# Kernel tuning notes

Hardware: AMD Instinct MI355X
Metric: run time of the kernel (lower is better)

## Reference

```python
import jax, jax.numpy as jnp
import numpy as np

NUM_CLASSES = 21
NUM_BOXES = 8732
BATCH = 128


def setup_inputs() -> dict:
    key = jax.random.key(0)
    k1, k2, k3, k4 = jax.random.split(key, 4)
    return {
        "loc_preds": jax.random.normal(k1, (BATCH, NUM_BOXES, 4), dtype=jnp.float32),
        "loc_targets": jax.random.normal(k2, (BATCH, NUM_BOXES, 4), dtype=jnp.float32),
        "conf_preds": jax.random.normal(k3, (BATCH, NUM_BOXES, NUM_CLASSES), dtype=jnp.float32),
        "label_targets": jax.random.randint(k4, (BATCH, NUM_BOXES), 0, NUM_CLASSES, dtype=jnp.int64),
    }


def reference(loc_preds, loc_targets, conf_preds, label_targets):
    n, num_boxes, _ = conf_preds.shape
    pos = label_targets > 0                                   # [n, B] matched boxes
    num_matched = jnp.sum(pos).astype(conf_preds.dtype)

    # --- localization loss: smooth L1 (beta=1) summed over positive boxes ---
    diff = loc_preds - loc_targets
    ad = jnp.abs(diff)
    sl1 = jnp.where(ad < 1.0, 0.5 * diff * diff, ad - 0.5)    # [n, B, 4]
    loc_loss = jnp.sum(jnp.where(pos[:, :, None], sl1, 0.0))

    # --- per-box CE for mining (original uses a single global max for logsumexp) ---
    x_max = jax.lax.stop_gradient(jnp.max(conf_preds))
    lse = jnp.log(jnp.sum(jnp.exp(conf_preds - x_max), axis=-1)) + x_max   # [n, B]
    gold = jnp.take_along_axis(conf_preds, label_targets[..., None], axis=-1)[..., 0]
    mining_loss = jnp.where(pos, -1.0, lse - gold)            # pos boxes forced lowest

    # --- hard negative mining: double argsort -> rank of each box's loss ---
    idx = jnp.argsort(-mining_loss, axis=1)                   # descending sort indices
    rank = jnp.argsort(idx, axis=1)                           # rank of each box
    num_pos = jnp.sum(pos.astype(jnp.int32), axis=1)          # [n]
    num_neg = jnp.minimum(3 * num_pos, num_boxes - 1)         # [n]
    neg = rank < num_neg[:, None]
    sel = pos | neg                                           # [n, B]

    # --- confidence loss: standard CE over selected boxes (F.cross_entropy) ---
    logp = jax.nn.log_softmax(conf_preds, axis=-1)
    ce = -jnp.take_along_axis(logp, label_targets[..., None], axis=-1)[..., 0]
    conf_loss = jnp.sum(jnp.where(sel, ce, 0.0))

    denom = jnp.maximum(num_matched, 1.0)
    return (loc_loss + conf_loss) / denom
```

## Files before the change

### kernel.cpp

```cpp
#include <hip/hip_runtime.h>

#define NB 8732
#define NC 21
#define BATCH 128
#define BX 35

#define WS_ROW (BATCH * BX * 4)

__device__ inline float wred_f(float v) {
#pragma unroll
    for (int o = 32; o > 0; o >>= 1) v += __shfl_down(v, o, 64);
    return v;
}

__global__ void __launch_bounds__(256)
kA(const float* __restrict__ locp, const float* __restrict__ loct,
   const float* __restrict__ conf, const int* __restrict__ lab,
   float* __restrict__ ws) {
    __shared__ float xb[4][1344];
    const int r = blockIdx.y;
    const int w = threadIdx.x >> 6;
    const int ln = threadIdx.x & 63;
    const int box0 = blockIdx.x * 256 + w * 64;

    float ceS = 0.f, pceS = 0.f, llS = 0.f, npS = 0.f;

    if (box0 < NB) {
        const int cnt = min(64, NB - box0);
        const size_t rowbase = (size_t)r * NB;
        const float* __restrict__ src = conf + (rowbase + box0) * (size_t)NC;

        int l = 0;
        float4 lp = {0.f, 0.f, 0.f, 0.f}, lt = {0.f, 0.f, 0.f, 0.f};
        if (ln < cnt) {
            const size_t box = rowbase + box0 + ln;
            l = lab[box];
            lp = *(const float4*)(locp + box * 4);
            lt = *(const float4*)(loct + box * 4);
        }

        if (cnt == 64) {
            float v[21];
#pragma unroll
            for (int j = 0; j < 21; j++) v[j] = src[64 * j + ln];
#pragma unroll
            for (int j = 0; j < 21; j++) xb[w][64 * j + ln] = v[j];
        } else {
            const int nflat = cnt * NC;
#pragma unroll
            for (int j = 0; j < 21; j++) {
                const int idx = 64 * j + ln;
                if (idx < nflat) xb[w][idx] = src[idx];
            }
        }
        asm volatile("s_waitcnt lgkmcnt(0)" ::: "memory");

        if (ln < cnt) {
            float c[21];
            const float* bp = &xb[w][21 * ln];
#pragma unroll
            for (int j = 0; j < 21; j++) c[j] = bp[j];
            float m = c[0];
#pragma unroll
            for (int j = 1; j < 21; j++) m = fmaxf(m, c[j]);
            float s = 0.f;
#pragma unroll
            for (int j = 0; j < 21; j++) s += __expf(c[j] - m);
            float gold = c[0];
#pragma unroll
            for (int j = 1; j < 21; j++) gold = (j == l) ? c[j] : gold;
            const float ce = m + __logf(s) - gold;
            ceS = ce;
            if (l > 0) {
                npS = 1.f;
                pceS = ce;
                float d, ad;
                d = lp.x - lt.x; ad = fabsf(d); llS += (ad < 1.f) ? 0.5f * d * d : ad - 0.5f;
                d = lp.y - lt.y; ad = fabsf(d); llS += (ad < 1.f) ? 0.5f * d * d : ad - 0.5f;
                d = lp.z - lt.z; ad = fabsf(d); llS += (ad < 1.f) ? 0.5f * d * d : ad - 0.5f;
                d = lp.w - lt.w; ad = fabsf(d); llS += (ad < 1.f) ? 0.5f * d * d : ad - 0.5f;
            }
        }
    }

    __shared__ float sr[4][4];
    float v0 = wred_f(ceS), v1 = wred_f(pceS), v2 = wred_f(llS), v3 = wred_f(npS);
    if (ln == 0) { sr[0][w] = v0; sr[1][w] = v1; sr[2][w] = v2; sr[3][w] = v3; }
    __syncthreads();
    if (threadIdx.x == 0) {
        float A = 0, B = 0, C = 0, D = 0;
#pragma unroll
        for (int k = 0; k < 4; k++) { A += sr[0][k]; B += sr[1][k]; C += sr[2][k]; D += sr[3][k]; }
        float* slot = ws + ((size_t)r * BX + blockIdx.x) * 4;
        slot[0] = A; slot[1] = B; slot[2] = C; slot[3] = D;
    }
}

__device__ inline float ce_for_box0(const float* __restrict__ cp) {
    float c[NC];
#pragma unroll
    for (int j = 0; j < NC; j++) c[j] = cp[j];
    float m = c[0];
#pragma unroll
    for (int j = 1; j < NC; j++) m = fmaxf(m, c[j]);
    float s = 0.f;
#pragma unroll
    for (int j = 0; j < NC; j++) s += __expf(c[j] - m);
    return m + __logf(s) - c[0];
}

__global__ void __launch_bounds__(256)
kB(const float* __restrict__ conf, const int* __restrict__ lab,
   float* __restrict__ ws) {
    const int r = blockIdx.x;
    __shared__ float srow[4];
    if (threadIdx.x < 64) {
        float a = 0, b = 0, c = 0, d = 0;
        if (threadIdx.x < BX) {
            const float4 p = *(const float4*)(ws + ((size_t)r * BX + threadIdx.x) * 4);
            a = p.x; b = p.y; c = p.z; d = p.w;
        }
        a = wred_f(a); b = wred_f(b); c = wred_f(c); d = wred_f(d);
        if (threadIdx.x == 0) { srow[0] = a; srow[1] = b; srow[2] = c; srow[3] = d; }
    }
    __syncthreads();
    const float row_ce = srow[0], row_pce = srow[1], row_ll = srow[2];
    const int np = (int)srow[3];
    const int K = min(3 * np, NB - 1);
    const int nneg = NB - np;

    float rowval;
    if (K >= nneg) {
        rowval = row_ce;
    } else if (K <= 0) {
        rowval = row_pce;
    } else {
        __shared__ unsigned key[NB];
        __shared__ unsigned hist[256];
        __shared__ unsigned sb[2];
        for (int i = threadIdx.x; i < NB; i += 256) {
            const size_t box = (size_t)r * NB + i;
            unsigned k = 0u;
            if (lab[box] == 0) {
                float ce = ce_for_box0(conf + box * (size_t)NC);
                k = __float_as_uint(fmaxf(ce, 0.f));
            }
            key[i] = k;
        }
        __syncthreads();
        unsigned prefix = 0;
        int Kr = K;
        for (int round = 3; round >= 0; --round) {
            const int sh = round * 8;
            const unsigned pmask = (round == 3) ? 0u : (0xFFFFFFFFu << (8 * (round + 1)));
            for (int b = threadIdx.x; b < 256; b += 256) hist[b] = 0;
            __syncthreads();
            for (int i = threadIdx.x; i < NB; i += 256) {
                const unsigned k = key[i];
                if ((k & pmask) == prefix) atomicAdd(&hist[(k >> sh) & 255u], 1u);
            }
            __syncthreads();
            if (threadIdx.x == 0) {
                unsigned cum = 0; int b = 255;
                for (; b > 0; --b) {
                    const unsigned h = hist[b];
                    if (cum + h >= (unsigned)Kr) break;
                    cum += h;
                }
                sb[0] = cum; sb[1] = (unsigned)b;
            }
            __syncthreads();
            Kr -= (int)sb[0];
            prefix |= (sb[1] << sh);
            __syncthreads();
        }
        float local = 0.f;
        for (int i = threadIdx.x; i < NB; i += 256) {
            const unsigned k = key[i];
            if (k > prefix) local += __uint_as_float(k);
        }
        __shared__ float sred[4];
        float v = wred_f(local);
        const int ww = threadIdx.x >> 6, lnn = threadIdx.x & 63;
        if (lnn == 0) sred[ww] = v;
        __syncthreads();
        rowval = row_pce + sred[0] + sred[1] + sred[2] + sred[3]
               + (float)Kr * __uint_as_float(prefix);
    }

    if (threadIdx.x == 0) {
        float* o = ws + WS_ROW + r * 4;
        o[0] = rowval; o[1] = row_ll; o[2] = srow[3];
    }
}

__global__ void __launch_bounds__(256)
kC(const float* __restrict__ ws, float* __restrict__ out) {
    float cf = 0.f, lc = 0.f, nm = 0.f;
    if (threadIdx.x < BATCH) {
        const float* o = ws + WS_ROW + threadIdx.x * 4;
        cf = o[0]; lc = o[1]; nm = o[2];
    }
    __shared__ float sf[4], sl[4], sn[4];
    float vc = wred_f(cf), vl = wred_f(lc), vn = wred_f(nm);
    const int w = threadIdx.x >> 6, ln = threadIdx.x & 63;
    if (ln == 0) { sf[w] = vc; sl[w] = vl; sn[w] = vn; }
    __syncthreads();
    if (threadIdx.x == 0) {
        const float CF = sf[0] + sf[1] + sf[2] + sf[3];
        const float LC = sl[0] + sl[1] + sl[2] + sl[3];
        const float NM = sn[0] + sn[1] + sn[2] + sn[3];
        out[0] = (LC + CF) / fmaxf(NM, 1.f);
    }
}

extern "C" void kernel_launch(void* const* d_in, const int* in_sizes, int n_in,
                              void* d_out, int out_size, void* d_ws, size_t ws_size,
                              hipStream_t stream) {
    const float* locp = (const float*)d_in[0];
    const float* loct = (const float*)d_in[1];
    const float* conf = (const float*)d_in[2];
    const int* lab = (const int*)d_in[3];
    float* out = (float*)d_out;
    float* ws = (float*)d_ws;

    hipLaunchKernelGGL(kA, dim3(BX, BATCH), dim3(256), 0, stream,
                       locp, loct, conf, lab, ws);
    hipLaunchKernelGGL(kB, dim3(BATCH), dim3(256), 0, stream, conf, lab, ws);
    hipLaunchKernelGGL(kC, dim3(1), dim3(256), 0, stream, ws, out);
}
```

Baseline: 176.2 us.

## Make kA persistent per row with double-buffered register prefetch of chunks

The grid of kA shrinks from 35 to 7 blocks per row. Each wave now loops over 64-box chunks with a stride of 28 waves, and it prefetches the next chunk's confidence, label and loc data into registers while the current chunk goes through shared memory and the CE computation. The goal is to hide global-load latency and cut per-block overhead and the number of partial sums kB must reduce. In exchange the kernel uses more registers, since launch_bounds(256,4) and two 21-float buffers raise spill risk, and the grid is smaller with only 896 blocks, so latency hiding depends on the software pipeline.

```diff
diff --git a/kernel.cpp b/kernel.cpp
--- a/kernel.cpp
+++ b/kernel.cpp
@@ -3,9 +3,10 @@
 #define NB 8732
 #define NC 21
 #define BATCH 128
-#define BX 35
-
-#define WS_ROW (BATCH * BX * 4)
+#define BXS 7
+#define WPR 28
+#define STRIDE (WPR * 64)
+#define WS_ROW (BATCH * BXS * 4)
 
 __device__ inline float wred_f(float v) {
 #pragma unroll
@@ -13,7 +14,7 @@
     return v;
 }
 
-__global__ void __launch_bounds__(256)
+__global__ void __launch_bounds__(256, 4)
 kA(const float* __restrict__ locp, const float* __restrict__ loct,
    const float* __restrict__ conf, const int* __restrict__ lab,
    float* __restrict__ ws) {
@@ -21,77 +22,116 @@
     const int r = blockIdx.y;
     const int w = threadIdx.x >> 6;
     const int ln = threadIdx.x & 63;
-    const int box0 = blockIdx.x * 256 + w * 64;
+    float* X = xb[w];
+    const int wid = blockIdx.x * 4 + w;
+    const size_t rowbase = (size_t)r * NB;
+    const float* __restrict__ crow = conf + rowbase * NC;
 
     float ceS = 0.f, pceS = 0.f, llS = 0.f, npS = 0.f;
 
-    if (box0 < NB) {
-        const int cnt = min(64, NB - box0);
-        const size_t rowbase = (size_t)r * NB;
-        const float* __restrict__ src = conf + (rowbase + box0) * (size_t)NC;
-
-        int l = 0;
-        float4 lp = {0.f, 0.f, 0.f, 0.f}, lt = {0.f, 0.f, 0.f, 0.f};
-        if (ln < cnt) {
-            const size_t box = rowbase + box0 + ln;
-            l = lab[box];
-            lp = *(const float4*)(locp + box * 4);
-            lt = *(const float4*)(loct + box * 4);
-        }
-
-        if (cnt == 64) {
-            float v[21];
-#pragma unroll
-            for (int j = 0; j < 21; j++) v[j] = src[64 * j + ln];
-#pragma unroll
-            for (int j = 0; j < 21; j++) xb[w][64 * j + ln] = v[j];
-        } else {
-            const int nflat = cnt * NC;
-#pragma unroll
-            for (int j = 0; j < 21; j++) {
-                const int idx = 64 * j + ln;
-                if (idx < nflat) xb[w][idx] = src[idx];
-            }
-        }
-        asm volatile("s_waitcnt lgkmcnt(0)" ::: "memory");
-
-        if (ln < cnt) {
-            float c[21];
-            const float* bp = &xb[w][21 * ln];
-#pragma unroll
-            for (int j = 0; j < 21; j++) c[j] = bp[j];
-            float m = c[0];
-#pragma unroll
-            for (int j = 1; j < 21; j++) m = fmaxf(m, c[j]);
-            float s = 0.f;
-#pragma unroll
-            for (int j = 0; j < 21; j++) s += __expf(c[j] - m);
-            float gold = c[0];
-#pragma unroll
-            for (int j = 1; j < 21; j++) gold = (j == l) ? c[j] : gold;
-            const float ce = m + __logf(s) - gold;
-            ceS = ce;
-            if (l > 0) {
-                npS = 1.f;
-                pceS = ce;
-                float d, ad;
-                d = lp.x - lt.x; ad = fabsf(d); llS += (ad < 1.f) ? 0.5f * d * d : ad - 0.5f;
-                d = lp.y - lt.y; ad = fabsf(d); llS += (ad < 1.f) ? 0.5f * d * d : ad - 0.5f;
-                d = lp.z - lt.z; ad = fabsf(d); llS += (ad < 1.f) ? 0.5f * d * d : ad - 0.5f;
-                d = lp.w - lt.w; ad = fabsf(d); llS += (ad < 1.f) ? 0.5f * d * d : ad - 0.5f;
-            }
-        }
+    float v[2][21];
+    int lv[2];
+    float4 lp[2], lt[2];
+
+#define LOADT(B, BOX0, CNT)                                                   \
+    {                                                                         \
+        const float* __restrict__ src = crow + (size_t)(BOX0) * NC;           \
+        if ((CNT) == 64) {                                                    \
+            _Pragma("unroll") for (int j = 0; j < 21; j++)                    \
+                v[B][j] = src[64 * j + ln];                                   \
+        } else {                                                              \
+            const int nflat = (CNT) * NC;                                     \
+            _Pragma("unroll") for (int j = 0; j < 21; j++) {                  \
+                const int idx = 64 * j + ln;                                  \
+                v[B][j] = (idx < nflat) ? src[idx] : 0.f;                     \
+            }                                                                 \
+        }                                                                     \
+        lv[B] = 0;                                                            \
+        if (ln < (CNT)) {                                                     \
+            const size_t box = rowbase + (BOX0) + ln;                         \
+            lv[B] = lab[box];                                                 \
+            lp[B] = *(const float4*)(locp + box * 4);                         \
+            lt[B] = *(const float4*)(loct + box * 4);                         \
+        }                                                                     \
+    }
+
+#define WLDS(B, CNT)                                                          \
+    {                                                                         \
+        if ((CNT) == 64) {                                                    \
+            _Pragma("unroll") for (int j = 0; j < 21; j++)                    \
+                X[64 * j + ln] = v[B][j];                                     \
+        } else {                                                              \
+            const int nflat = (CNT) * NC;                                     \
+            _Pragma("unroll") for (int j = 0; j < 21; j++) {                  \
+                const int idx = 64 * j + ln;                                  \
+                if (idx < nflat) X[idx] = v[B][j];                            \
+            }                                                                 \
+        }                                                                     \
+    }
+
+#define CONSUME(B, CNT)                                                       \
+    {                                                                         \
+        asm volatile("s_waitcnt lgkmcnt(0)" ::: "memory");                    \
+        if (ln < (CNT)) {                                                     \
+            float c[21];                                                      \
+            const float* bp = &X[21 * ln];                                    \
+            _Pragma("unroll") for (int j = 0; j < 21; j++) c[j] = bp[j];      \
+            float m = c[0];                                                   \
+            _Pragma("unroll") for (int j = 1; j < 21; j++) m = fmaxf(m, c[j]);\
+            float s = 0.f;                                                    \
+            _Pragma("unroll") for (int j = 0; j < 21; j++)                    \
+                s += __expf(c[j] - m);                                        \
+            const int l = lv[B];                                              \
+            float gold = c[0];                                                \
+            _Pragma("unroll") for (int j = 1; j < 21; j++)                    \
+                gold = (j == l) ? c[j] : gold;                                \
+            const float ce = m + __logf(s) - gold;                            \
+            ceS += ce;                                                        \
+            if (l > 0) {                                                      \
+                npS += 1.f; pceS += ce;                                       \
+                const float4 P = lp[B], T = lt[B];                            \
+                float d, ad;                                                  \
+                d = P.x - T.x; ad = fabsf(d); llS += (ad < 1.f) ? 0.5f * d * d : ad - 0.5f; \
+                d = P.y - T.y; ad = fabsf(d); llS += (ad < 1.f) ? 0.5f * d * d : ad - 0.5f; \
+                d = P.z - T.z; ad = fabsf(d); llS += (ad < 1.f) ? 0.5f * d * d : ad - 0.5f; \
+                d = P.w - T.w; ad = fabsf(d); llS += (ad < 1.f) ? 0.5f * d * d : ad - 0.5f; \
+            }                                                                 \
+        }                                                                     \
+    }
+
+    int b0 = wid * 64;
+    int c0 = min(64, NB - b0);
+    LOADT(0, b0, c0)
+    int b1 = b0 + STRIDE;
+    bool have1 = (b1 < NB);
+    int c1 = have1 ? min(64, NB - b1) : 0;
+
+    for (;;) {
+        WLDS(0, c0)
+        if (have1) LOADT(1, b1, c1)
+        CONSUME(0, c0)
+        if (!have1) break;
+        b0 = b1 + STRIDE;
+        const bool have0 = (b0 < NB);
+        c0 = have0 ? min(64, NB - b0) : 0;
+        WLDS(1, c1)
+        if (have0) LOADT(0, b0, c0)
+        CONSUME(1, c1)
+        if (!have0) break;
+        b1 = b0 + STRIDE;
+        have1 = (b1 < NB);
+        c1 = have1 ? min(64, NB - b1) : 0;
     }
 
     __shared__ float sr[4][4];
-    float v0 = wred_f(ceS), v1 = wred_f(pceS), v2 = wred_f(llS), v3 = wred_f(npS);
-    if (ln == 0) { sr[0][w] = v0; sr[1][w] = v1; sr[2][w] = v2; sr[3][w] = v3; }
+    float r0 = wred_f(ceS), r1 = wred_f(pceS), r2 = wred_f(llS), r3 = wred_f(npS);
+    if (ln == 0) { sr[0][w] = r0; sr[1][w] = r1; sr[2][w] = r2; sr[3][w] = r3; }
     __syncthreads();
     if (threadIdx.x == 0) {
         float A = 0, B = 0, C = 0, D = 0;
 #pragma unroll
         for (int k = 0; k < 4; k++) { A += sr[0][k]; B += sr[1][k]; C += sr[2][k]; D += sr[3][k]; }
-        float* slot = ws + ((size_t)r * BX + blockIdx.x) * 4;
+        float* slot = ws + ((size_t)r * BXS + blockIdx.x) * 4;
         slot[0] = A; slot[1] = B; slot[2] = C; slot[3] = D;
     }
 }
@@ -116,8 +156,8 @@
     __shared__ float srow[4];
     if (threadIdx.x < 64) {
         float a = 0, b = 0, c = 0, d = 0;
-        if (threadIdx.x < BX) {
-            const float4 p = *(const float4*)(ws + ((size_t)r * BX + threadIdx.x) * 4);
+        if (threadIdx.x < BXS) {
+            const float4 p = *(const float4*)(ws + ((size_t)r * BXS + threadIdx.x) * 4);
             a = p.x; b = p.y; c = p.z; d = p.w;
         }
         a = wred_f(a); b = wred_f(b); c = wred_f(c); d = wred_f(d);
@@ -180,9 +220,9 @@
             if (k > prefix) local += __uint_as_float(k);
         }
         __shared__ float sred[4];
-        float v = wred_f(local);
+        float vv = wred_f(local);
         const int ww = threadIdx.x >> 6, lnn = threadIdx.x & 63;
-        if (lnn == 0) sred[ww] = v;
+        if (lnn == 0) sred[ww] = vv;
         __syncthreads();
         rowval = row_pce + sred[0] + sred[1] + sred[2] + sred[3]
                + (float)Kr * __uint_as_float(prefix);
@@ -224,7 +264,7 @@
     float* out = (float*)d_out;
     float* ws = (float*)d_ws;
 
-    hipLaunchKernelGGL(kA, dim3(BX, BATCH), dim3(256), 0, stream,
+    hipLaunchKernelGGL(kA, dim3(BXS, BATCH), dim3(256), 0, stream,
                        locp, loct, conf, lab, ws);
     hipLaunchKernelGGL(kB, dim3(BATCH), dim3(256), 0, stream, conf, lab, ws);
     hipLaunchKernelGGL(kC, dim3(1), dim3(256), 0, stream, ws, out);
```

Measured after the change: 194.1 us. +10.1%, slower.

## Double-buffer conf tiles via global_load_lds in persistent single-wave kA blocks

Applied to the files above, without the earlier changes.

Rewrites the first-pass kernel so each 64-thread block walks a strided set of 64-box tiles. Conf, loc and label data go straight from global memory into LDS through global_load_lds, into two buffers so the next tile's loads overlap the current tile's softmax and CE math. This removes the register staging step and replaces the 256-thread block shape with persistent single-wave blocks that pipeline their loads. The cost is fewer resident waves, hand-counted vmcnt waits that depend on how many loads each ISSUE emits, and a separate scalar path for the 28-box tail.

```diff
diff --git a/kernel.cpp b/kernel.cpp
--- a/kernel.cpp
+++ b/kernel.cpp
@@ -3,9 +3,9 @@
 #define NB 8732
 #define NC 21
 #define BATCH 128
-#define BX 35
-
-#define WS_ROW (BATCH * BX * 4)
+#define WPR 20
+#define NFULL 136
+#define WS_ROW (BATCH * WPR * 4)
 
 __device__ inline float wred_f(float v) {
 #pragma unroll
@@ -13,86 +13,109 @@
     return v;
 }
 
-__global__ void __launch_bounds__(256)
+__device__ __forceinline__ void gl_lds16(const void* g, void* l) {
+    __builtin_amdgcn_global_load_lds((const __attribute__((address_space(1))) void*)g,
+                                     (__attribute__((address_space(3))) void*)l, 16, 0, 0);
+}
+__device__ __forceinline__ void gl_lds4(const void* g, void* l) {
+    __builtin_amdgcn_global_load_lds((const __attribute__((address_space(1))) void*)g,
+                                     (__attribute__((address_space(3))) void*)l, 4, 0, 0);
+}
+
+__device__ __forceinline__ void box_accum(const float c[21], int l,
+                                          float4 lp, float4 lt,
+                                          float& ceS, float& pceS, float& llS, float& npS) {
+    float m = c[0];
+#pragma unroll
+    for (int j = 1; j < 21; j++) m = fmaxf(m, c[j]);
+    float s = 0.f;
+#pragma unroll
+    for (int j = 0; j < 21; j++) s += __expf(c[j] - m);
+    float gold = c[0];
+#pragma unroll
+    for (int j = 1; j < 21; j++) gold = (j == l) ? c[j] : gold;
+    const float ce = m + __logf(s) - gold;
+    ceS += ce;
+    if (l > 0) {
+        npS += 1.f; pceS += ce;
+        float d, ad;
+        d = lp.x - lt.x; ad = fabsf(d); llS += (ad < 1.f) ? 0.5f * d * d : ad - 0.5f;
+        d = lp.y - lt.y; ad = fabsf(d); llS += (ad < 1.f) ? 0.5f * d * d : ad - 0.5f;
+        d = lp.z - lt.z; ad = fabsf(d); llS += (ad < 1.f) ? 0.5f * d * d : ad - 0.5f;
+        d = lp.w - lt.w; ad = fabsf(d); llS += (ad < 1.f) ? 0.5f * d * d : ad - 0.5f;
+    }
+}
+
+__global__ void __launch_bounds__(64)
 kA(const float* __restrict__ locp, const float* __restrict__ loct,
    const float* __restrict__ conf, const int* __restrict__ lab,
    float* __restrict__ ws) {
-    __shared__ float xb[4][1344];
+    __shared__ float buf[2][1920];
     const int r = blockIdx.y;
-    const int w = threadIdx.x >> 6;
-    const int ln = threadIdx.x & 63;
-    const int box0 = blockIdx.x * 256 + w * 64;
+    const int wid = blockIdx.x;
+    const int ln = threadIdx.x;
+    const size_t rowbase = (size_t)r * NB;
 
     float ceS = 0.f, pceS = 0.f, llS = 0.f, npS = 0.f;
 
-    if (box0 < NB) {
-        const int cnt = min(64, NB - box0);
-        const size_t rowbase = (size_t)r * NB;
-        const float* __restrict__ src = conf + (rowbase + box0) * (size_t)NC;
-
-        int l = 0;
-        float4 lp = {0.f, 0.f, 0.f, 0.f}, lt = {0.f, 0.f, 0.f, 0.f};
-        if (ln < cnt) {
-            const size_t box = rowbase + box0 + ln;
-            l = lab[box];
-            lp = *(const float4*)(locp + box * 4);
-            lt = *(const float4*)(loct + box * 4);
-        }
-
-        if (cnt == 64) {
-            float v[21];
-#pragma unroll
-            for (int j = 0; j < 21; j++) v[j] = src[64 * j + ln];
-#pragma unroll
-            for (int j = 0; j < 21; j++) xb[w][64 * j + ln] = v[j];
+#define ISSUE(B, BOX0)                                                        \
+    {                                                                         \
+        const char* gc = (const char*)(conf + (rowbase + (size_t)(BOX0)) * NC); \
+        _Pragma("unroll") for (int k = 0; k < 5; k++)                         \
+            gl_lds16(gc + k * 1024 + ln * 16, &buf[B][k * 256]);              \
+        if (ln < 16) gl_lds16(gc + 5120 + ln * 16, &buf[B][1280]);            \
+        gl_lds16((const char*)(locp + (rowbase + (BOX0)) * 4) + ln * 16,      \
+                 &buf[B][1344]);                                              \
+        gl_lds16((const char*)(loct + (rowbase + (BOX0)) * 4) + ln * 16,      \
+                 &buf[B][1600]);                                              \
+        gl_lds4((const char*)(lab + rowbase + (BOX0)) + ln * 4,               \
+                &buf[B][1856]);                                               \
+    }
+
+#define CONSUME(B)                                                            \
+    {                                                                         \
+        float c[21];                                                          \
+        _Pragma("unroll") for (int j = 0; j < 21; j++)                        \
+            c[j] = buf[B][21 * ln + j];                                       \
+        const int l = ((const int*)(&buf[B][1856]))[ln];                      \
+        const float4 lp = ((const float4*)(&buf[B][1344]))[ln];               \
+        const float4 lt = ((const float4*)(&buf[B][1600]))[ln];               \
+        box_accum(c, l, lp, lt, ceS, pceS, llS, npS);                         \
+    }
+
+    const int ntiles = (NFULL - 1 - wid) / WPR + 1;
+
+    ISSUE(0, wid * 64)
+    for (int i = 0; i < ntiles; i++) {
+        const bool more = (i + 1) < ntiles;
+        if (more) {
+            const int nbox = (wid + (i + 1) * WPR) * 64;
+            if ((i & 1) == 0) ISSUE(1, nbox) else ISSUE(0, nbox)
+            asm volatile("s_waitcnt vmcnt(9)" ::: "memory");
         } else {
-            const int nflat = cnt * NC;
-#pragma unroll
-            for (int j = 0; j < 21; j++) {
-                const int idx = 64 * j + ln;
-                if (idx < nflat) xb[w][idx] = src[idx];
-            }
-        }
-        asm volatile("s_waitcnt lgkmcnt(0)" ::: "memory");
-
-        if (ln < cnt) {
+            asm volatile("s_waitcnt vmcnt(0)" ::: "memory");
+        }
+        if ((i & 1) == 0) CONSUME(0) else CONSUME(1)
+    }
+
+    if (wid == (NFULL % WPR)) {
+        if (ln < NB - NFULL * 64) {
+            const size_t box = rowbase + NFULL * 64 + ln;
+            const float* cp = conf + box * (size_t)NC;
             float c[21];
-            const float* bp = &xb[w][21 * ln];
-#pragma unroll
-            for (int j = 0; j < 21; j++) c[j] = bp[j];
-            float m = c[0];
-#pragma unroll
-            for (int j = 1; j < 21; j++) m = fmaxf(m, c[j]);
-            float s = 0.f;
-#pragma unroll
-            for (int j = 0; j < 21; j++) s += __expf(c[j] - m);
-            float gold = c[0];
-#pragma unroll
-            for (int j = 1; j < 21; j++) gold = (j == l) ? c[j] : gold;
-            const float ce = m + __logf(s) - gold;
-            ceS = ce;
-            if (l > 0) {
-                npS = 1.f;
-                pceS = ce;
-                float d, ad;
-                d = lp.x - lt.x; ad = fabsf(d); llS += (ad < 1.f) ? 0.5f * d * d : ad - 0.5f;
-                d = lp.y - lt.y; ad = fabsf(d); llS += (ad < 1.f) ? 0.5f * d * d : ad - 0.5f;
-                d = lp.z - lt.z; ad = fabsf(d); llS += (ad < 1.f) ? 0.5f * d * d : ad - 0.5f;
-                d = lp.w - lt.w; ad = fabsf(d); llS += (ad < 1.f) ? 0.5f * d * d : ad - 0.5f;
-            }
-        }
-    }
-
-    __shared__ float sr[4][4];
-    float v0 = wred_f(ceS), v1 = wred_f(pceS), v2 = wred_f(llS), v3 = wred_f(npS);
-    if (ln == 0) { sr[0][w] = v0; sr[1][w] = v1; sr[2][w] = v2; sr[3][w] = v3; }
-    __syncthreads();
-    if (threadIdx.x == 0) {
-        float A = 0, B = 0, C = 0, D = 0;
-#pragma unroll
-        for (int k = 0; k < 4; k++) { A += sr[0][k]; B += sr[1][k]; C += sr[2][k]; D += sr[3][k]; }
-        float* slot = ws + ((size_t)r * BX + blockIdx.x) * 4;
-        slot[0] = A; slot[1] = B; slot[2] = C; slot[3] = D;
+#pragma unroll
+            for (int j = 0; j < 21; j++) c[j] = cp[j];
+            const int l = lab[box];
+            const float4 lp = *(const float4*)(locp + box * 4);
+            const float4 lt = *(const float4*)(loct + box * 4);
+            box_accum(c, l, lp, lt, ceS, pceS, llS, npS);
+        }
+    }
+
+    float A = wred_f(ceS), Bv = wred_f(pceS), C = wred_f(llS), D = wred_f(npS);
+    if (ln == 0) {
+        float4* slot = (float4*)(ws + ((size_t)r * WPR + wid) * 4);
+        *slot = make_float4(A, Bv, C, D);
     }
 }
 
@@ -116,8 +139,8 @@
     __shared__ float srow[4];
     if (threadIdx.x < 64) {
         float a = 0, b = 0, c = 0, d = 0;
-        if (threadIdx.x < BX) {
-            const float4 p = *(const float4*)(ws + ((size_t)r * BX + threadIdx.x) * 4);
+        if (threadIdx.x < WPR) {
+            const float4 p = *(const float4*)(ws + ((size_t)r * WPR + threadIdx.x) * 4);
             a = p.x; b = p.y; c = p.z; d = p.w;
         }
         a = wred_f(a); b = wred_f(b); c = wred_f(c); d = wred_f(d);
@@ -180,9 +203,9 @@
             if (k > prefix) local += __uint_as_float(k);
         }
         __shared__ float sred[4];
-        float v = wred_f(local);
+        float vv = wred_f(local);
         const int ww = threadIdx.x >> 6, lnn = threadIdx.x & 63;
-        if (lnn == 0) sred[ww] = v;
+        if (lnn == 0) sred[ww] = vv;
         __syncthreads();
         rowval = row_pce + sred[0] + sred[1] + sred[2] + sred[3]
                + (float)Kr * __uint_as_float(prefix);
@@ -224,7 +247,7 @@
     float* out = (float*)d_out;
     float* ws = (float*)d_ws;
 
-    hipLaunchKernelGGL(kA, dim3(BX, BATCH), dim3(256), 0, stream,
+    hipLaunchKernelGGL(kA, dim3(WPR, BATCH), dim3(64), 0, stream,
                        locp, loct, conf, lab, ws);
     hipLaunchKernelGGL(kB, dim3(BATCH), dim3(256), 0, stream, conf, lab, ws);
     hipLaunchKernelGGL(kC, dim3(1), dim3(256), 0, stream, ws, out);
```

After: 179.3 us. Within noise of the previous version (+1.8%).
